# Kernel tuning notes

Hardware: AMD Instinct MI355X
Metric: run time of the kernel (lower is better)

The kernel has to match this reference:

```python
import jax, jax.numpy as jnp
import numpy as np
from jax import lax

THR = 1.0
BETA = 0.9
SLOPE = 25.0  # fast_sigmoid surrogate slope
N_JOINTS = 6

@jax.custom_vjp
def spike_fn(x):
    # Heaviside forward, fast_sigmoid surrogate backward (snntorch surrogate.fast_sigmoid)
    return (x > 0).astype(x.dtype)

def _spike_fwd(x):
    return spike_fn(x), x

def _spike_bwd(x, g):
    return (g / (SLOPE * jnp.abs(x) + 1.0) ** 2,)

spike_fn.defvjp(_spike_fwd, _spike_bwd)

def lif(cur, mem):
    # snntorch Leaky, reset_mechanism='subtract': reset from previous mem (detached)
    reset = lax.stop_gradient(spike_fn(mem - THR))
    mem = BETA * mem + cur - reset * THR
    spk = spike_fn(mem - THR)
    return spk, mem

def rate_encode(data, u):
    # data: (B, F), u: (T, B, F) uniform[0,1) -> binary spikes (T, B, F)
    dmin = jnp.min(data, axis=1, keepdims=True)
    dmax = jnp.max(data, axis=1, keepdims=True)
    rng = dmax - dmin
    rng = jnp.where(rng == 0, jnp.ones_like(rng), rng)
    norm = (data - dmin) / rng
    prob = jnp.clip(100.0 * norm * 0.001, 0.0, 1.0)  # max_rate=100, dt=0.001
    return (u < prob[None]).astype(jnp.float32)

def conv1x1(x, W, b):
    # x: (B, Cin, H, 1), W: (Cout, Cin, 1, 1)
    y = lax.conv_general_dilated(x, W, (1, 1), 'VALID',
                                 dimension_numbers=('NCHW', 'OIHW', 'NCHW'))
    return y + b[None, :, None, None]

def setup_inputs() -> dict:
    key = jax.random.key(0)
    ks = jax.random.split(key, 16)
    B, T, n = 8192, 200, N_JOINTS
    inp = {
        'x':  jax.random.normal(ks[0], (B, 3 * n), jnp.float32),
        'u1': jax.random.uniform(ks[1], (T, B, 2 * n), jnp.float32),
        'u2': jax.random.uniform(ks[2], (T, B, n), jnp.float32),
        'u3': jax.random.uniform(ks[3], (T, B, n), jnp.float32),
        'W1': jax.random.normal(ks[4], (256, 12), jnp.float32) * 0.2,
        'b1': jax.random.normal(ks[5], (256,), jnp.float32) * 0.05,
        'W2': jax.random.normal(ks[6], (256, 256), jnp.float32) * 0.06,
        'b2': jax.random.normal(ks[7], (256,), jnp.float32) * 0.05,
        'W3': jax.random.normal(ks[8], (6, 256), jnp.float32) * 0.06,
        'b3': jax.random.normal(ks[9], (6,), jnp.float32) * 0.05,
        'Wc1': jax.random.normal(ks[10], (32, 3, 1, 1), jnp.float32) * 0.5,
        'bc1': jax.random.normal(ks[11], (32,), jnp.float32) * 0.05,
        'Wc2': jax.random.normal(ks[12], (64, 32, 1, 1), jnp.float32) * 0.15,
        'bc2': jax.random.normal(ks[13], (64,), jnp.float32) * 0.05,
        'WA': jax.random.normal(ks[14], (1, 64), jnp.float32) * 0.12,
    }
    return inp

def reference(x, u1, u2, u3, W1, b1, W2, b2, W3, b3, Wc1, bc1, Wc2, bc2, WA):
    n = N_JOINTS
    B = x.shape[0]
    spk_in = rate_encode(x[:, :2 * n], u1)        # (T, B, 2n)
    spk_thdot = rate_encode(x[:, n:2 * n], u2)    # (T, B, n)
    spk_thdot2 = rate_encode(x[:, 2 * n:], u3)    # (T, B, n)

    mem1 = jnp.zeros((B, 256), jnp.float32)
    mem2 = jnp.zeros((B, 256), jnp.float32)
    mem3 = jnp.zeros((B, n), jnp.float32)
    mem4 = jnp.zeros((B, 32, n, 1), jnp.float32)
    conv_out0 = jnp.zeros((B, 64, n, 1), jnp.float32)

    def step(carry, inp):
        m1, m2, m3, m4, _ = carry
        s_in, s_td, s_td2 = inp
        spk1, m1 = lif(s_in @ W1.T + b1, m1)
        spk2, m2 = lif(spk1 @ W2.T + b2, m2)
        spk3, m3 = lif(spk2 @ W3.T + b3, m3)
        spk_conv = jnp.stack([s_td, spk3, s_td2], axis=1)[..., None]  # (B,3,n,1)
        cur4 = conv1x1(spk_conv, Wc1, bc1)  # maxpool1 with k=1 is identity
        spk4, m4 = lif(cur4, m4)
        conv_out = conv1x1(spk4, Wc2, bc2)  # maxpool2 with k=1 is identity
        return (m1, m2, m3, m4, conv_out), None

    (_, _, _, _, conv_out), _ = lax.scan(step, (mem1, mem2, mem3, mem4, conv_out0),
                                         (spk_in, spk_thdot, spk_thdot2))
    # c.T: out_a/b/c = fc_A(conv_out[:, :, i, 0]) for i in 0..2, no bias
    c_t = jnp.einsum('bcm,c->bm', conv_out[:, :, :3, 0], WA[0])  # (B, 3)
    return c_t
```

## Files before the change

### kernel.cpp

```cpp
#include <hip/hip_runtime.h>
#include <cstdint>
#include <cstddef>

typedef unsigned long long u64;

__global__ void prep_weights(const float* __restrict__ W2, const float* __restrict__ Wc2,
                             const float* __restrict__ bc2, const float* __restrict__ WA,
                             float* __restrict__ Wt2f, double* __restrict__ wEff,
                             double* __restrict__ bEff)
{
  int id = blockIdx.x * 256 + (int)threadIdx.x;
  if (id < 65536){ int i = id >> 8, j = id & 255; Wt2f[(i<<8)+j] = W2[j*256+i]; }
  else if (id < 65792){ Wt2f[id] = 0.0f; }
  if (id < 32){ double s = 0.0; for (int c=0;c<64;c++) s += (double)WA[c]*(double)Wc2[c*32+id]; wEff[id] = s; }
  if (id == 32){ double s = 0.0; for (int c=0;c<64;c++) s += (double)WA[c]*(double)bc2[c]; *bEff = s; }
}

__global__ void prep_probs(const float* __restrict__ x, double* __restrict__ probs, int B)
{
  int b = blockIdx.x, k = (int)threadIdx.x;
  if (b >= B || k >= 24) return;
  double* pb = probs + (size_t)b*24;
  if (k >= 18){ pb[k] = -1.0; return; }
  int fk, g0, gn;
  if (k < 12){ fk = k;          g0 = 0;  gn = 12; }
  else if (k < 15){ fk = 6+(k-12);  g0 = 6;  gn = 6; }
  else           { fk = 12+(k-15); g0 = 12; gn = 6; }
  const float* xb = x + (size_t)b*18;
  double mn = (double)xb[g0], mx = mn;
  for (int f = 1; f < gn; f++){ double v = (double)xb[g0+f]; mn = fmin(mn, v); mx = fmax(mx, v); }
  double rng = mx - mn; if (rng == 0.0) rng = 1.0;
  double norm = ((double)xb[fk] - mn) / rng;
  double p = (100.0 * norm) * 0.001;
  p = fmin(fmax(p, 0.0), 1.0);
  pb[k] = p;
}

__global__ void prep_enc(const float* __restrict__ u1, const float* __restrict__ u2,
                         const float* __restrict__ u3, const double* __restrict__ probs,
                         unsigned* __restrict__ encT, int B, int T)
{
  int b = blockIdx.x * blockDim.x + (int)threadIdx.x;
  int t = blockIdx.y;
  if (b >= B) return;
  if (t >= T){ encT[(size_t)b*(T+2) + t] = 0u; return; }
  const double* pb = probs + (size_t)b*24;
  size_t r = (size_t)t * B + b;
  const float* a1 = u1 + r*12;
  const float* a2 = u2 + r*6;
  const float* a3 = u3 + r*6;
  unsigned e = 0;
  #pragma unroll
  for (int k = 0; k < 12; k++) if ((double)a1[k] < pb[k])    e |= (1u << k);
  #pragma unroll
  for (int h = 0; h < 3; h++)  if ((double)a2[h] < pb[12+h]) e |= (1u << (12+h));
  #pragma unroll
  for (int h = 0; h < 3; h++)  if ((double)a3[h] < pb[15+h]) e |= (1u << (15+h));
  encT[(size_t)b*(T+2) + t] = e;
}

__global__ __launch_bounds__(256) void snn_main(
    const unsigned* __restrict__ encT,
    const float* __restrict__ b1, const float* __restrict__ b2, const float* __restrict__ b3,
    const float* __restrict__ W1, const float* __restrict__ W3,
    const float* __restrict__ Wc1, const float* __restrict__ bc1,
    const float* __restrict__ Wt2f,
    const double* __restrict__ wEff, const double* __restrict__ bEff,
    float* __restrict__ out, int B, int T)
{
  __shared__ __align__(16) float s_w1[12*256];
  __shared__ __align__(16) float s_w3[257*4];

  const int tid  = (int)threadIdx.x;
  const int lane = tid & 63;
  const int wid  = tid >> 6;
  const int b = blockIdx.x * 4 + wid;
  const int l4 = lane << 2;
  const int lcl = (lane < 3) ? lane : 3;

  for (int i = tid; i < 3072; i += 256){ int k = i >> 8, j = i & 255; s_w1[i] = W1[j*12+k]; }
  for (int i = tid; i < 1028; i += 256){
    int r = i >> 2, c = i & 3;
    s_w3[i] = (r < 256 && c < 3) ? W3[c*256 + r] : 0.0f;
  }
  __syncthreads();
  if (b >= B) return;

  const float4 b1f = *(const float4*)(b1 + l4);
  const float4 b2f = *(const float4*)(b2 + l4);
  const double b1d0=b1f.x, b1d1=b1f.y, b1d2=b1f.z, b1d3=b1f.w;
  const double b2d0=b2f.x, b2d1=b2f.y, b2d2=b2f.z, b2d3=b2f.w;
  const double b3d = (lane < 3) ? (double)b3[lane] : 0.0;
  double wc1b=0.0, wEd=0.0, pre0=0.0, pre1=0.0, pre2=0.0, pre3=0.0;
  if (lane < 32){
    double wa = (double)Wc1[lane*3+0];
    wc1b      = (double)Wc1[lane*3+1];
    double wc = (double)Wc1[lane*3+2];
    double bd = (double)bc1[lane];
    wEd  = wEff[lane];
    pre0 = bd;
    pre1 = bd + wa;
    pre2 = bd + wc;
    pre3 = bd + wa + wc;
  }

  double m10=0,m11=0,m12=0,m13=0;
  double m20=0,m21=0,m22=0,m23=0;
  double m3v=0;
  double m40=0,m41=0,m42=0;
  bool sp20=false,sp21=false,sp22=false,sp23=false;
  bool sp3v=false;
  bool sp40=false,sp41=false,sp42=false;

  const unsigned* encTb = encT + (size_t)b * (T + 2);

  unsigned e_cur = __builtin_amdgcn_readfirstlane(encTb[0]);
  unsigned e_nx  = __builtin_amdgcn_readfirstlane(encTb[1]);
  double ca0=b1d0, ca1=b1d1, ca2=b1d2, ca3=b1d3;
  {
    unsigned w = e_cur & 0xFFFu;
    while (w){
      int k = __builtin_ctz(w); w &= w-1;
      const float4 r = *(const float4*)&s_w1[(k<<8) + l4];
      ca0 += (double)r.x; ca1 += (double)r.y; ca2 += (double)r.z; ca3 += (double)r.w;
    }
  }

  for (int t = 0; t < T; t++){
    m10 = fma(0.9, m10, ca0);
    m11 = fma(0.9, m11, ca1);
    m12 = fma(0.9, m12, ca2);
    m13 = fma(0.9, m13, ca3);
    const bool sp10 = m10 > 1.0; u64 w0 = __ballot(sp10);
    const bool sp11 = m11 > 1.0; u64 w1 = __ballot(sp11);
    const bool sp12 = m12 > 1.0; u64 w2 = __ballot(sp12);
    const bool sp13 = m13 > 1.0; u64 w3m = __ballot(sp13);

    int i0 = w0  ? (((int)__builtin_ctzll(w0) <<2)|0) : 256;  w0  &= w0 -1;
    int i1 = w1  ? (((int)__builtin_ctzll(w1) <<2)|1) : 256;  w1  &= w1 -1;
    int i2 = w2  ? (((int)__builtin_ctzll(w2) <<2)|2) : 256;  w2  &= w2 -1;
    int i3 = w3m ? (((int)__builtin_ctzll(w3m)<<2)|3) : 256;  w3m &= w3m-1;
    const float4 g0 = *(const float4*)(Wt2f + ((size_t)i0<<8) + l4);
    const float4 g1 = *(const float4*)(Wt2f + ((size_t)i1<<8) + l4);
    const float4 g2 = *(const float4*)(Wt2f + ((size_t)i2<<8) + l4);
    const float4 g3 = *(const float4*)(Wt2f + ((size_t)i3<<8) + l4);

    const unsigned e_n2 = encTb[t+2];

    ca0 = (sp10 ? -1.0 : 0.0) + b1d0;
    ca1 = (sp11 ? -1.0 : 0.0) + b1d1;
    ca2 = (sp12 ? -1.0 : 0.0) + b1d2;
    ca3 = (sp13 ? -1.0 : 0.0) + b1d3;
    {
      unsigned w = e_nx & 0xFFFu;
      while (w){
        int k = __builtin_ctz(w); w &= w-1;
        const float4 r = *(const float4*)&s_w1[(k<<8) + l4];
        ca0 += (double)r.x; ca1 += (double)r.y; ca2 += (double)r.z; ca3 += (double)r.w;
      }
    }

    double c0 = (sp20 ? -1.0 : 0.0) + b2d0;
    double c1 = (sp21 ? -1.0 : 0.0) + b2d1;
    double c2 = (sp22 ? -1.0 : 0.0) + b2d2;
    double c3 = (sp23 ? -1.0 : 0.0) + b2d3;
    if (i0 != 256){ c0 += (double)g0.x; c1 += (double)g0.y; c2 += (double)g0.z; c3 += (double)g0.w; }
    if (i1 != 256){ c0 += (double)g1.x; c1 += (double)g1.y; c2 += (double)g1.z; c3 += (double)g1.w; }
    if (i2 != 256){ c0 += (double)g2.x; c1 += (double)g2.y; c2 += (double)g2.z; c3 += (double)g2.w; }
    if (i3 != 256){ c0 += (double)g3.x; c1 += (double)g3.y; c2 += (double)g3.z; c3 += (double)g3.w; }

    while (w0 | w1 | w2 | w3m){
      int j0 = w0  ? (((int)__builtin_ctzll(w0) <<2)|0) : 256;  w0  &= w0 -1;
      int j1 = w1  ? (((int)__builtin_ctzll(w1) <<2)|1) : 256;  w1  &= w1 -1;
      int j2 = w2  ? (((int)__builtin_ctzll(w2) <<2)|2) : 256;  w2  &= w2 -1;
      int j3 = w3m ? (((int)__builtin_ctzll(w3m)<<2)|3) : 256;  w3m &= w3m-1;
      const float4 h0 = *(const float4*)(Wt2f + ((size_t)j0<<8) + l4);
      const float4 h1 = *(const float4*)(Wt2f + ((size_t)j1<<8) + l4);
      const float4 h2 = *(const float4*)(Wt2f + ((size_t)j2<<8) + l4);
      const float4 h3 = *(const float4*)(Wt2f + ((size_t)j3<<8) + l4);
      if (j0 != 256){ c0 += (double)h0.x; c1 += (double)h0.y; c2 += (double)h0.z; c3 += (double)h0.w; }
      if (j1 != 256){ c0 += (double)h1.x; c1 += (double)h1.y; c2 += (double)h1.z; c3 += (double)h1.w; }
      if (j2 != 256){ c0 += (double)h2.x; c1 += (double)h2.y; c2 += (double)h2.z; c3 += (double)h2.w; }
      if (j3 != 256){ c0 += (double)h3.x; c1 += (double)h3.y; c2 += (double)h3.z; c3 += (double)h3.w; }
    }

    m20 = fma(0.9, m20, c0);
    m21 = fma(0.9, m21, c1);
    m22 = fma(0.9, m22, c2);
    m23 = fma(0.9, m23, c3);
    sp20 = m20 > 1.0; u64 v0 = __ballot(sp20);
    sp21 = m21 > 1.0; u64 v1 = __ballot(sp21);
    sp22 = m22 > 1.0; u64 v2 = __ballot(sp22);
    sp23 = m23 > 1.0; u64 v3 = __ballot(sp23);

    double cl3 = (sp3v ? -1.0 : 0.0) + b3d;
    while (v0 | v1 | v2 | v3){
      int j0 = v0 ? (((int)__builtin_ctzll(v0)<<2)|0) : 256;  v0 &= v0-1;
      int j1 = v1 ? (((int)__builtin_ctzll(v1)<<2)|1) : 256;  v1 &= v1-1;
      int j2 = v2 ? (((int)__builtin_ctzll(v2)<<2)|2) : 256;  v2 &= v2-1;
      int j3 = v3 ? (((int)__builtin_ctzll(v3)<<2)|3) : 256;  v3 &= v3-1;
      if (j0 != 256) cl3 += (double)s_w3[(j0<<2) + lcl];
      if (j1 != 256) cl3 += (double)s_w3[(j1<<2) + lcl];
      if (j2 != 256) cl3 += (double)s_w3[(j2<<2) + lcl];
      if (j3 != 256) cl3 += (double)s_w3[(j3<<2) + lcl];
    }
    m3v = fma(0.9, m3v, cl3);
    sp3v = m3v > 1.0;
    const unsigned s3 = (unsigned)(__ballot((lane < 3) && sp3v) & 7ull);

    const unsigned td  = (e_cur >> 12) & 7u;
    const unsigned td2 = (e_cur >> 15) & 7u;
    {
      double cur, t1, t2;
      t1 = (td2 & 1u) ? pre2 : pre0;  t2 = (td2 & 1u) ? pre3 : pre1;
      cur = (td & 1u) ? t2 : t1;
      if (s3 & 1u) cur += wc1b;
      cur += sp40 ? -1.0 : 0.0;
      m40 = fma(0.9, m40, cur); sp40 = m40 > 1.0;
      t1 = (td2 & 2u) ? pre2 : pre0;  t2 = (td2 & 2u) ? pre3 : pre1;
      cur = (td & 2u) ? t2 : t1;
      if (s3 & 2u) cur += wc1b;
      cur += sp41 ? -1.0 : 0.0;
      m41 = fma(0.9, m41, cur); sp41 = m41 > 1.0;
      t1 = (td2 & 4u) ? pre2 : pre0;  t2 = (td2 & 4u) ? pre3 : pre1;
      cur = (td & 4u) ? t2 : t1;
      if (s3 & 4u) cur += wc1b;
      cur += sp42 ? -1.0 : 0.0;
      m42 = fma(0.9, m42, cur); sp42 = m42 > 1.0;
    }

    e_cur = e_nx;
    e_nx  = __builtin_amdgcn_readfirstlane(e_n2);
  }

  double o0 = sp40 ? wEd : 0.0;
  double o1 = sp41 ? wEd : 0.0;
  double o2 = sp42 ? wEd : 0.0;
  for (int off = 32; off > 0; off >>= 1){
    o0 += __shfl_xor(o0, off, 64);
    o1 += __shfl_xor(o1, off, 64);
    o2 += __shfl_xor(o2, off, 64);
  }
  if (lane == 0){
    const double be = *bEff;
    out[b*3+0] = (float)(o0 + be);
    out[b*3+1] = (float)(o1 + be);
    out[b*3+2] = (float)(o2 + be);
  }
}

extern "C" void kernel_launch(void* const* d_in, const int* in_sizes, int n_in,
                              void* d_out, int out_size, void* d_ws, size_t ws_size,
                              hipStream_t stream)
{
  const float* x   = (const float*)d_in[0];
  const float* u1  = (const float*)d_in[1];
  const float* u2  = (const float*)d_in[2];
  const float* u3  = (const float*)d_in[3];
  const float* W1  = (const float*)d_in[4];
  const float* b1  = (const float*)d_in[5];
  const float* W2  = (const float*)d_in[6];
  const float* b2  = (const float*)d_in[7];
  const float* W3  = (const float*)d_in[8];
  const float* b3  = (const float*)d_in[9];
  const float* Wc1 = (const float*)d_in[10];
  const float* bc1 = (const float*)d_in[11];
  const float* Wc2 = (const float*)d_in[12];
  const float* bc2 = (const float*)d_in[13];
  const float* WA  = (const float*)d_in[14];
  float* out = (float*)d_out;

  const int B = in_sizes[0] / 18;
  const int T = in_sizes[1] / (B * 12);

  char* ws = (char*)d_ws;
  float*  Wt2f  = (float*)(ws + 0);
  double* wEff  = (double*)(ws + 263168);
  double* bEff  = (double*)(ws + 263424);
  double* probs = (double*)(ws + 263432);
  unsigned* encT= (unsigned*)(ws + 263432 + (size_t)B*24*8);

  hipLaunchKernelGGL(prep_weights, dim3(257), dim3(256), 0, stream,
                     W2, Wc2, bc2, WA, Wt2f, wEff, bEff);
  hipLaunchKernelGGL(prep_probs, dim3(B), dim3(64), 0, stream, x, probs, B);
  hipLaunchKernelGGL(prep_enc, dim3((B+255)/256, T+2), dim3(256), 0, stream,
                     u1, u2, u3, probs, encT, B, T);
  hipLaunchKernelGGL(snn_main, dim3((B+3)/4), dim3(256), 0, stream,
                     encT, b1, b2, b3, W1, W3, Wc1, bc1, Wt2f, wEff, bEff, out, B, T);
}
```

Measured before the change: 684.1 us.

## Split each batch row across two wavefronts with LDS ballot exchange

Each batch sample now runs on two wavefronts of a 128-thread block, and each lane owns two hidden neurons instead of four. The wavefronts swap their spike ballots through shared memory and block barriers twice per timestep, and only wave 0 evaluates layers 3 and 4. W1 and W3 transposes move into the prep kernel and are read from global memory instead of per-block LDS copies. This shortens the per-wave serial dependency chain and raises parallelism, at the cost of two __syncthreads per step and duplicated spike-list walks in both waves.

```diff
diff --git a/kernel.cpp b/kernel.cpp
--- a/kernel.cpp
+++ b/kernel.cpp
@@ -4,14 +4,24 @@
 
 typedef unsigned long long u64;
 
-__global__ void prep_weights(const float* __restrict__ W2, const float* __restrict__ Wc2,
+__device__ inline u64 rfl64(u64 v){
+  unsigned lo = __builtin_amdgcn_readfirstlane((unsigned)v);
+  unsigned hi = __builtin_amdgcn_readfirstlane((unsigned)(v >> 32));
+  return ((u64)hi << 32) | lo;
+}
+
+__global__ void prep_weights(const float* __restrict__ W1, const float* __restrict__ W2,
+                             const float* __restrict__ W3, const float* __restrict__ Wc2,
                              const float* __restrict__ bc2, const float* __restrict__ WA,
-                             float* __restrict__ Wt2f, double* __restrict__ wEff,
+                             float* __restrict__ Wt1g, float* __restrict__ Wt2f,
+                             float* __restrict__ Wt3f, double* __restrict__ wEff,
                              double* __restrict__ bEff)
 {
   int id = blockIdx.x * 256 + (int)threadIdx.x;
   if (id < 65536){ int i = id >> 8, j = id & 255; Wt2f[(i<<8)+j] = W2[j*256+i]; }
   else if (id < 65792){ Wt2f[id] = 0.0f; }
+  if (id < 3072){ int k = id >> 8, j = id & 255; Wt1g[(k<<8)+j] = W1[j*12+k]; }
+  if (id < 1028){ int r = id >> 2, c = id & 3; Wt3f[id] = (r < 256 && c < 3) ? W3[c*256+r] : 0.0f; }
   if (id < 32){ double s = 0.0; for (int c=0;c<64;c++) s += (double)WA[c]*(double)Wc2[c*32+id]; wEff[id] = s; }
   if (id == 32){ double s = 0.0; for (int c=0;c<64;c++) s += (double)WA[c]*(double)bc2[c]; *bEff = s; }
 }
@@ -59,40 +69,30 @@
   encT[(size_t)b*(T+2) + t] = e;
 }
 
-__global__ __launch_bounds__(256) void snn_main(
+__global__ __launch_bounds__(128, 8) void snn_main(
     const unsigned* __restrict__ encT,
     const float* __restrict__ b1, const float* __restrict__ b2, const float* __restrict__ b3,
-    const float* __restrict__ W1, const float* __restrict__ W3,
     const float* __restrict__ Wc1, const float* __restrict__ bc1,
-    const float* __restrict__ Wt2f,
+    const float* __restrict__ Wt1g, const float* __restrict__ Wt2f, const float* __restrict__ Wt3f,
     const double* __restrict__ wEff, const double* __restrict__ bEff,
     float* __restrict__ out, int B, int T)
 {
-  __shared__ __align__(16) float s_w1[12*256];
-  __shared__ __align__(16) float s_w3[257*4];
+  __shared__ u64 xb1[2][2];
+  __shared__ u64 xb2[2];
 
   const int tid  = (int)threadIdx.x;
   const int lane = tid & 63;
-  const int wid  = tid >> 6;
-  const int b = blockIdx.x * 4 + wid;
-  const int l4 = lane << 2;
-  const int lcl = (lane < 3) ? lane : 3;
-
-  for (int i = tid; i < 3072; i += 256){ int k = i >> 8, j = i & 255; s_w1[i] = W1[j*12+k]; }
-  for (int i = tid; i < 1028; i += 256){
-    int r = i >> 2, c = i & 3;
-    s_w3[i] = (r < 256 && c < 3) ? W3[c*256 + r] : 0.0f;
-  }
-  __syncthreads();
+  const int wv   = tid >> 6;
+  const int b    = blockIdx.x;
   if (b >= B) return;
-
-  const float4 b1f = *(const float4*)(b1 + l4);
-  const float4 b2f = *(const float4*)(b2 + l4);
-  const double b1d0=b1f.x, b1d1=b1f.y, b1d2=b1f.z, b1d3=b1f.w;
-  const double b2d0=b2f.x, b2d1=b2f.y, b2d2=b2f.z, b2d3=b2f.w;
+  const int j2   = (wv << 7) + (lane << 1);
+  const int lcl  = (lane < 3) ? lane : 3;
+
+  const float2 b1f = *(const float2*)(b1 + j2);
+  const float2 b2f = *(const float2*)(b2 + j2);
   const double b3d = (lane < 3) ? (double)b3[lane] : 0.0;
   double wc1b=0.0, wEd=0.0, pre0=0.0, pre1=0.0, pre2=0.0, pre3=0.0;
-  if (lane < 32){
+  if (wv == 0 && lane < 32){
     double wa = (double)Wc1[lane*3+0];
     wc1b      = (double)Wc1[lane*3+1];
     double wc = (double)Wc1[lane*3+2];
@@ -104,126 +104,132 @@
     pre3 = bd + wa + wc;
   }
 
-  double m10=0,m11=0,m12=0,m13=0;
-  double m20=0,m21=0,m22=0,m23=0;
+  double m10=0,m11=0;
+  double m20=0,m21=0;
   double m3v=0;
   double m40=0,m41=0,m42=0;
-  bool sp20=false,sp21=false,sp22=false,sp23=false;
+  bool sp20=false,sp21=false;
   bool sp3v=false;
   bool sp40=false,sp41=false,sp42=false;
 
   const unsigned* encTb = encT + (size_t)b * (T + 2);
-
   unsigned e_cur = __builtin_amdgcn_readfirstlane(encTb[0]);
   unsigned e_nx  = __builtin_amdgcn_readfirstlane(encTb[1]);
-  double ca0=b1d0, ca1=b1d1, ca2=b1d2, ca3=b1d3;
+
+  double ca0 = (double)b1f.x, ca1 = (double)b1f.y;
   {
     unsigned w = e_cur & 0xFFFu;
     while (w){
       int k = __builtin_ctz(w); w &= w-1;
-      const float4 r = *(const float4*)&s_w1[(k<<8) + l4];
-      ca0 += (double)r.x; ca1 += (double)r.y; ca2 += (double)r.z; ca3 += (double)r.w;
+      const float2 r = *(const float2*)(Wt1g + (k<<8) + j2);
+      ca0 += (double)r.x; ca1 += (double)r.y;
     }
   }
 
   for (int t = 0; t < T; t++){
     m10 = fma(0.9, m10, ca0);
     m11 = fma(0.9, m11, ca1);
-    m12 = fma(0.9, m12, ca2);
-    m13 = fma(0.9, m13, ca3);
-    const bool sp10 = m10 > 1.0; u64 w0 = __ballot(sp10);
-    const bool sp11 = m11 > 1.0; u64 w1 = __ballot(sp11);
-    const bool sp12 = m12 > 1.0; u64 w2 = __ballot(sp12);
-    const bool sp13 = m13 > 1.0; u64 w3m = __ballot(sp13);
-
-    int i0 = w0  ? (((int)__builtin_ctzll(w0) <<2)|0) : 256;  w0  &= w0 -1;
-    int i1 = w1  ? (((int)__builtin_ctzll(w1) <<2)|1) : 256;  w1  &= w1 -1;
-    int i2 = w2  ? (((int)__builtin_ctzll(w2) <<2)|2) : 256;  w2  &= w2 -1;
-    int i3 = w3m ? (((int)__builtin_ctzll(w3m)<<2)|3) : 256;  w3m &= w3m-1;
-    const float4 g0 = *(const float4*)(Wt2f + ((size_t)i0<<8) + l4);
-    const float4 g1 = *(const float4*)(Wt2f + ((size_t)i1<<8) + l4);
-    const float4 g2 = *(const float4*)(Wt2f + ((size_t)i2<<8) + l4);
-    const float4 g3 = *(const float4*)(Wt2f + ((size_t)i3<<8) + l4);
+    const bool sp10 = m10 > 1.0;
+    const bool sp11 = m11 > 1.0;
+    const u64 bb0 = __ballot(sp10);
+    const u64 bb1 = __ballot(sp11);
+
+    if (lane < 2) xb1[wv][lane] = lane ? bb1 : bb0;
+    __syncthreads();
+    const u64 o0m = rfl64(xb1[wv^1][0]);
+    const u64 o1m = rfl64(xb1[wv^1][1]);
+    u64 q0, q1, q2, q3;
+    if (wv == 0){ q0 = bb0; q1 = bb1; q2 = o0m; q3 = o1m; }
+    else        { q0 = o0m; q1 = o1m; q2 = bb0; q3 = bb1; }
+
+    int i0 = q0 ? (int)(__builtin_ctzll(q0)<<1)           : 256;  q0 &= q0-1;
+    int i1 = q1 ? (int)((__builtin_ctzll(q1)<<1)|1)       : 256;  q1 &= q1-1;
+    int i2 = q2 ? (int)((__builtin_ctzll(q2)<<1)+128)     : 256;  q2 &= q2-1;
+    int i3 = q3 ? (int)(((__builtin_ctzll(q3)<<1)|1)+128) : 256;  q3 &= q3-1;
+    const float2 g0 = *(const float2*)(Wt2f + ((size_t)i0<<8) + j2);
+    const float2 g1 = *(const float2*)(Wt2f + ((size_t)i1<<8) + j2);
+    const float2 g2 = *(const float2*)(Wt2f + ((size_t)i2<<8) + j2);
+    const float2 g3 = *(const float2*)(Wt2f + ((size_t)i3<<8) + j2);
 
     const unsigned e_n2 = encTb[t+2];
 
-    ca0 = (sp10 ? -1.0 : 0.0) + b1d0;
-    ca1 = (sp11 ? -1.0 : 0.0) + b1d1;
-    ca2 = (sp12 ? -1.0 : 0.0) + b1d2;
-    ca3 = (sp13 ? -1.0 : 0.0) + b1d3;
+    ca0 = (sp10 ? -1.0 : 0.0) + (double)b1f.x;
+    ca1 = (sp11 ? -1.0 : 0.0) + (double)b1f.y;
     {
       unsigned w = e_nx & 0xFFFu;
       while (w){
         int k = __builtin_ctz(w); w &= w-1;
-        const float4 r = *(const float4*)&s_w1[(k<<8) + l4];
-        ca0 += (double)r.x; ca1 += (double)r.y; ca2 += (double)r.z; ca3 += (double)r.w;
+        const float2 r = *(const float2*)(Wt1g + (k<<8) + j2);
+        ca0 += (double)r.x; ca1 += (double)r.y;
       }
     }
 
-    double c0 = (sp20 ? -1.0 : 0.0) + b2d0;
-    double c1 = (sp21 ? -1.0 : 0.0) + b2d1;
-    double c2 = (sp22 ? -1.0 : 0.0) + b2d2;
-    double c3 = (sp23 ? -1.0 : 0.0) + b2d3;
-    if (i0 != 256){ c0 += (double)g0.x; c1 += (double)g0.y; c2 += (double)g0.z; c3 += (double)g0.w; }
-    if (i1 != 256){ c0 += (double)g1.x; c1 += (double)g1.y; c2 += (double)g1.z; c3 += (double)g1.w; }
-    if (i2 != 256){ c0 += (double)g2.x; c1 += (double)g2.y; c2 += (double)g2.z; c3 += (double)g2.w; }
-    if (i3 != 256){ c0 += (double)g3.x; c1 += (double)g3.y; c2 += (double)g3.z; c3 += (double)g3.w; }
-
-    while (w0 | w1 | w2 | w3m){
-      int j0 = w0  ? (((int)__builtin_ctzll(w0) <<2)|0) : 256;  w0  &= w0 -1;
-      int j1 = w1  ? (((int)__builtin_ctzll(w1) <<2)|1) : 256;  w1  &= w1 -1;
-      int j2 = w2  ? (((int)__builtin_ctzll(w2) <<2)|2) : 256;  w2  &= w2 -1;
-      int j3 = w3m ? (((int)__builtin_ctzll(w3m)<<2)|3) : 256;  w3m &= w3m-1;
-      const float4 h0 = *(const float4*)(Wt2f + ((size_t)j0<<8) + l4);
-      const float4 h1 = *(const float4*)(Wt2f + ((size_t)j1<<8) + l4);
-      const float4 h2 = *(const float4*)(Wt2f + ((size_t)j2<<8) + l4);
-      const float4 h3 = *(const float4*)(Wt2f + ((size_t)j3<<8) + l4);
-      if (j0 != 256){ c0 += (double)h0.x; c1 += (double)h0.y; c2 += (double)h0.z; c3 += (double)h0.w; }
-      if (j1 != 256){ c0 += (double)h1.x; c1 += (double)h1.y; c2 += (double)h1.z; c3 += (double)h1.w; }
-      if (j2 != 256){ c0 += (double)h2.x; c1 += (double)h2.y; c2 += (double)h2.z; c3 += (double)h2.w; }
-      if (j3 != 256){ c0 += (double)h3.x; c1 += (double)h3.y; c2 += (double)h3.z; c3 += (double)h3.w; }
+    double c0 = (sp20 ? -1.0 : 0.0) + (double)b2f.x;
+    double c1 = (sp21 ? -1.0 : 0.0) + (double)b2f.y;
+    if (i0 != 256){ c0 += (double)g0.x; c1 += (double)g0.y; }
+    if (i1 != 256){ c0 += (double)g1.x; c1 += (double)g1.y; }
+    if (i2 != 256){ c0 += (double)g2.x; c1 += (double)g2.y; }
+    if (i3 != 256){ c0 += (double)g3.x; c1 += (double)g3.y; }
+
+    while (q0 | q1 | q2 | q3){
+      int j0 = q0 ? (int)(__builtin_ctzll(q0)<<1)           : 256;  q0 &= q0-1;
+      int j1 = q1 ? (int)((__builtin_ctzll(q1)<<1)|1)       : 256;  q1 &= q1-1;
+      int j2i= q2 ? (int)((__builtin_ctzll(q2)<<1)+128)     : 256;  q2 &= q2-1;
+      int j3 = q3 ? (int)(((__builtin_ctzll(q3)<<1)|1)+128) : 256;  q3 &= q3-1;
+      const float2 h0 = *(const float2*)(Wt2f + ((size_t)j0 <<8) + j2);
+      const float2 h1 = *(const float2*)(Wt2f + ((size_t)j1 <<8) + j2);
+      const float2 h2 = *(const float2*)(Wt2f + ((size_t)j2i<<8) + j2);
+      const float2 h3 = *(const float2*)(Wt2f + ((size_t)j3 <<8) + j2);
+      if (j0 != 256){ c0 += (double)h0.x; c1 += (double)h0.y; }
+      if (j1 != 256){ c0 += (double)h1.x; c1 += (double)h1.y; }
+      if (j2i!= 256){ c0 += (double)h2.x; c1 += (double)h2.y; }
+      if (j3 != 256){ c0 += (double)h3.x; c1 += (double)h3.y; }
     }
 
     m20 = fma(0.9, m20, c0);
     m21 = fma(0.9, m21, c1);
-    m22 = fma(0.9, m22, c2);
-    m23 = fma(0.9, m23, c3);
-    sp20 = m20 > 1.0; u64 v0 = __ballot(sp20);
-    sp21 = m21 > 1.0; u64 v1 = __ballot(sp21);
-    sp22 = m22 > 1.0; u64 v2 = __ballot(sp22);
-    sp23 = m23 > 1.0; u64 v3 = __ballot(sp23);
-
-    double cl3 = (sp3v ? -1.0 : 0.0) + b3d;
-    while (v0 | v1 | v2 | v3){
-      int j0 = v0 ? (((int)__builtin_ctzll(v0)<<2)|0) : 256;  v0 &= v0-1;
-      int j1 = v1 ? (((int)__builtin_ctzll(v1)<<2)|1) : 256;  v1 &= v1-1;
-      int j2 = v2 ? (((int)__builtin_ctzll(v2)<<2)|2) : 256;  v2 &= v2-1;
-      int j3 = v3 ? (((int)__builtin_ctzll(v3)<<2)|3) : 256;  v3 &= v3-1;
-      if (j0 != 256) cl3 += (double)s_w3[(j0<<2) + lcl];
-      if (j1 != 256) cl3 += (double)s_w3[(j1<<2) + lcl];
-      if (j2 != 256) cl3 += (double)s_w3[(j2<<2) + lcl];
-      if (j3 != 256) cl3 += (double)s_w3[(j3<<2) + lcl];
-    }
-    m3v = fma(0.9, m3v, cl3);
-    sp3v = m3v > 1.0;
-    const unsigned s3 = (unsigned)(__ballot((lane < 3) && sp3v) & 7ull);
-
-    const unsigned td  = (e_cur >> 12) & 7u;
-    const unsigned td2 = (e_cur >> 15) & 7u;
-    {
-      double cur, t1, t2;
-      t1 = (td2 & 1u) ? pre2 : pre0;  t2 = (td2 & 1u) ? pre3 : pre1;
-      cur = (td & 1u) ? t2 : t1;
+    sp20 = m20 > 1.0;
+    sp21 = m21 > 1.0;
+    const u64 vb0 = __ballot(sp20);
+    const u64 vb1 = __ballot(sp21);
+
+    if (wv == 1 && lane < 2) xb2[lane] = lane ? vb1 : vb0;
+    __syncthreads();
+
+    if (wv == 0){
+      u64 v0 = vb0, v1 = vb1;
+      u64 v2 = rfl64(xb2[0]);
+      u64 v3 = rfl64(xb2[1]);
+      double cl3 = (sp3v ? -1.0 : 0.0) + b3d;
+      while (v0 | v1 | v2 | v3){
+        int j0 = v0 ? (int)(__builtin_ctzll(v0)<<1)           : 256;  v0 &= v0-1;
+        int j1 = v1 ? (int)((__builtin_ctzll(v1)<<1)|1)       : 256;  v1 &= v1-1;
+        int j2i= v2 ? (int)((__builtin_ctzll(v2)<<1)+128)     : 256;  v2 &= v2-1;
+        int j3 = v3 ? (int)(((__builtin_ctzll(v3)<<1)|1)+128) : 256;  v3 &= v3-1;
+        if (j0 != 256) cl3 += (double)Wt3f[(j0 <<2) + lcl];
+        if (j1 != 256) cl3 += (double)Wt3f[(j1 <<2) + lcl];
+        if (j2i!= 256) cl3 += (double)Wt3f[(j2i<<2) + lcl];
+        if (j3 != 256) cl3 += (double)Wt3f[(j3 <<2) + lcl];
+      }
+      m3v = fma(0.9, m3v, cl3);
+      sp3v = m3v > 1.0;
+      const unsigned s3 = (unsigned)(__ballot((lane < 3) && sp3v) & 7ull);
+
+      const unsigned td  = (e_cur >> 12) & 7u;
+      const unsigned td2 = (e_cur >> 15) & 7u;
+      double cur, t1v, t2v;
+      t1v = (td2 & 1u) ? pre2 : pre0;  t2v = (td2 & 1u) ? pre3 : pre1;
+      cur = (td & 1u) ? t2v : t1v;
       if (s3 & 1u) cur += wc1b;
       cur += sp40 ? -1.0 : 0.0;
       m40 = fma(0.9, m40, cur); sp40 = m40 > 1.0;
-      t1 = (td2 & 2u) ? pre2 : pre0;  t2 = (td2 & 2u) ? pre3 : pre1;
-      cur = (td & 2u) ? t2 : t1;
+      t1v = (td2 & 2u) ? pre2 : pre0;  t2v = (td2 & 2u) ? pre3 : pre1;
+      cur = (td & 2u) ? t2v : t1v;
       if (s3 & 2u) cur += wc1b;
       cur += sp41 ? -1.0 : 0.0;
       m41 = fma(0.9, m41, cur); sp41 = m41 > 1.0;
-      t1 = (td2 & 4u) ? pre2 : pre0;  t2 = (td2 & 4u) ? pre3 : pre1;
-      cur = (td & 4u) ? t2 : t1;
+      t1v = (td2 & 4u) ? pre2 : pre0;  t2v = (td2 & 4u) ? pre3 : pre1;
+      cur = (td & 4u) ? t2v : t1v;
       if (s3 & 4u) cur += wc1b;
       cur += sp42 ? -1.0 : 0.0;
       m42 = fma(0.9, m42, cur); sp42 = m42 > 1.0;
@@ -233,19 +239,21 @@
     e_nx  = __builtin_amdgcn_readfirstlane(e_n2);
   }
 
-  double o0 = sp40 ? wEd : 0.0;
-  double o1 = sp41 ? wEd : 0.0;
-  double o2 = sp42 ? wEd : 0.0;
-  for (int off = 32; off > 0; off >>= 1){
-    o0 += __shfl_xor(o0, off, 64);
-    o1 += __shfl_xor(o1, off, 64);
-    o2 += __shfl_xor(o2, off, 64);
-  }
-  if (lane == 0){
-    const double be = *bEff;
-    out[b*3+0] = (float)(o0 + be);
-    out[b*3+1] = (float)(o1 + be);
-    out[b*3+2] = (float)(o2 + be);
+  if (wv == 0){
+    double o0 = sp40 ? wEd : 0.0;
+    double o1 = sp41 ? wEd : 0.0;
+    double o2 = sp42 ? wEd : 0.0;
+    for (int off = 32; off > 0; off >>= 1){
+      o0 += __shfl_xor(o0, off, 64);
+      o1 += __shfl_xor(o1, off, 64);
+      o2 += __shfl_xor(o2, off, 64);
+    }
+    if (lane == 0){
+      const double be = *bEff;
+      out[b*3+0] = (float)(o0 + be);
+      out[b*3+1] = (float)(o1 + be);
+      out[b*3+2] = (float)(o2 + be);
+    }
   }
 }
 
@@ -275,16 +283,18 @@
 
   char* ws = (char*)d_ws;
   float*  Wt2f  = (float*)(ws + 0);
-  double* wEff  = (double*)(ws + 263168);
-  double* bEff  = (double*)(ws + 263424);
-  double* probs = (double*)(ws + 263432);
-  unsigned* encT= (unsigned*)(ws + 263432 + (size_t)B*24*8);
+  float*  Wt1g  = (float*)(ws + 263168);
+  float*  Wt3f  = (float*)(ws + 275456);
+  double* wEff  = (double*)(ws + 279576);
+  double* bEff  = (double*)(ws + 279832);
+  double* probs = (double*)(ws + 279840);
+  unsigned* encT= (unsigned*)(ws + 279840 + (size_t)B*24*8);
 
   hipLaunchKernelGGL(prep_weights, dim3(257), dim3(256), 0, stream,
-                     W2, Wc2, bc2, WA, Wt2f, wEff, bEff);
+                     W1, W2, W3, Wc2, bc2, WA, Wt1g, Wt2f, Wt3f, wEff, bEff);
   hipLaunchKernelGGL(prep_probs, dim3(B), dim3(64), 0, stream, x, probs, B);
   hipLaunchKernelGGL(prep_enc, dim3((B+255)/256, T+2), dim3(256), 0, stream,
                      u1, u2, u3, probs, encT, B, T);
-  hipLaunchKernelGGL(snn_main, dim3((B+3)/4), dim3(256), 0, stream,
-                     encT, b1, b2, b3, W1, W3, Wc1, bc1, Wt2f, wEff, bEff, out, B, T);
-}
+  hipLaunchKernelGGL(snn_main, dim3(B), dim3(128), 0, stream,
+                     encT, b1, b2, b3, Wc1, bc1, Wt1g, Wt2f, Wt3f, wEff, bEff, out, B, T);
+}
```

Result: slower. 2.002 ms (+192.6%).

## Process two batch rows per wavefront to interleave independent recurrences

Applied to the files above, without the earlier changes.

Each wavefront now simulates two batch rows (rA and rA+half) at once, interleaving their layer updates and the gathers from the transposed W2 so independent memory loads and double-precision FMAs can overlap within one serial time loop. This targets the latency-bound dependency chain of the per-row recurrence. In exchange it roughly doubles register pressure and halves the number of wavefronts launched, which can lower occupancy. The merged gather loop runs until the row with more spikes is done, so the other row's slots sit idle.

```diff
diff --git a/kernel.cpp b/kernel.cpp
--- a/kernel.cpp
+++ b/kernel.cpp
@@ -74,7 +74,8 @@
   const int tid  = (int)threadIdx.x;
   const int lane = tid & 63;
   const int wid  = tid >> 6;
-  const int b = blockIdx.x * 4 + wid;
+  const int half = (B + 1) >> 1;
+  const int rA = blockIdx.x * 4 + wid;
   const int l4 = lane << 2;
   const int lcl = (lane < 3) ? lane : 3;
 
@@ -84,12 +85,12 @@
     s_w3[i] = (r < 256 && c < 3) ? W3[c*256 + r] : 0.0f;
   }
   __syncthreads();
-  if (b >= B) return;
+  if (rA >= half) return;
+  const int rB = rA + half;
+  const bool hasB = rB < B;
 
   const float4 b1f = *(const float4*)(b1 + l4);
   const float4 b2f = *(const float4*)(b2 + l4);
-  const double b1d0=b1f.x, b1d1=b1f.y, b1d2=b1f.z, b1d3=b1f.w;
-  const double b2d0=b2f.x, b2d1=b2f.y, b2d2=b2f.z, b2d3=b2f.w;
   const double b3d = (lane < 3) ? (double)b3[lane] : 0.0;
   double wc1b=0.0, wEd=0.0, pre0=0.0, pre1=0.0, pre2=0.0, pre3=0.0;
   if (lane < 32){
@@ -98,154 +99,210 @@
     double wc = (double)Wc1[lane*3+2];
     double bd = (double)bc1[lane];
     wEd  = wEff[lane];
-    pre0 = bd;
-    pre1 = bd + wa;
-    pre2 = bd + wc;
-    pre3 = bd + wa + wc;
-  }
-
-  double m10=0,m11=0,m12=0,m13=0;
-  double m20=0,m21=0,m22=0,m23=0;
-  double m3v=0;
-  double m40=0,m41=0,m42=0;
-  bool sp20=false,sp21=false,sp22=false,sp23=false;
-  bool sp3v=false;
-  bool sp40=false,sp41=false,sp42=false;
-
-  const unsigned* encTb = encT + (size_t)b * (T + 2);
-
-  unsigned e_cur = __builtin_amdgcn_readfirstlane(encTb[0]);
-  unsigned e_nx  = __builtin_amdgcn_readfirstlane(encTb[1]);
-  double ca0=b1d0, ca1=b1d1, ca2=b1d2, ca3=b1d3;
-  {
-    unsigned w = e_cur & 0xFFFu;
-    while (w){
-      int k = __builtin_ctz(w); w &= w-1;
-      const float4 r = *(const float4*)&s_w1[(k<<8) + l4];
-      ca0 += (double)r.x; ca1 += (double)r.y; ca2 += (double)r.z; ca3 += (double)r.w;
-    }
-  }
+    pre0 = bd; pre1 = bd + wa; pre2 = bd + wc; pre3 = bd + wa + wc;
+  }
+
+  double m10A=0,m11A=0,m12A=0,m13A=0, m20A=0,m21A=0,m22A=0,m23A=0, m3A=0, m40A=0,m41A=0,m42A=0;
+  double m10B=0,m11B=0,m12B=0,m13B=0, m20B=0,m21B=0,m22B=0,m23B=0, m3B=0, m40B=0,m41B=0,m42B=0;
+  bool s20A=false,s21A=false,s22A=false,s23A=false, s3A=false, s40A=false,s41A=false,s42A=false;
+  bool s20B=false,s21B=false,s22B=false,s23B=false, s3B=false, s40B=false,s41B=false,s42B=false;
+
+  const unsigned* ebA = encT + (size_t)rA * (T + 2);
+  const unsigned* ebB = encT + (size_t)(hasB ? rB : 0) * (T + 2);
+  unsigned eAc = __builtin_amdgcn_readfirstlane(ebA[0]);
+  unsigned eAn = __builtin_amdgcn_readfirstlane(ebA[1]);
+  unsigned eBc = __builtin_amdgcn_readfirstlane(ebB[0]);
+  unsigned eBn = __builtin_amdgcn_readfirstlane(ebB[1]);
+
+#define L1G(EMASK, CA0, CA1, CA2, CA3) { unsigned w = (EMASK) & 0xFFFu; \
+    while (w){ int k = __builtin_ctz(w); w &= w-1; \
+      const float4 r = *(const float4*)&s_w1[(k<<8) + l4]; \
+      CA0 += (double)r.x; CA1 += (double)r.y; CA2 += (double)r.z; CA3 += (double)r.w; } }
+
+  double caA0=(double)b1f.x, caA1=(double)b1f.y, caA2=(double)b1f.z, caA3=(double)b1f.w;
+  double caB0=caA0, caB1=caA1, caB2=caA2, caB3=caA3;
+  L1G(eAc, caA0, caA1, caA2, caA3)
+  L1G(eBc, caB0, caB1, caB2, caB3)
+
+#define SLOT(Wm, CW, DST) { DST = (Wm) ? (((int)__builtin_ctzll(Wm)<<2)|(CW)) : 256; Wm &= (Wm)-1; }
 
   for (int t = 0; t < T; t++){
-    m10 = fma(0.9, m10, ca0);
-    m11 = fma(0.9, m11, ca1);
-    m12 = fma(0.9, m12, ca2);
-    m13 = fma(0.9, m13, ca3);
-    const bool sp10 = m10 > 1.0; u64 w0 = __ballot(sp10);
-    const bool sp11 = m11 > 1.0; u64 w1 = __ballot(sp11);
-    const bool sp12 = m12 > 1.0; u64 w2 = __ballot(sp12);
-    const bool sp13 = m13 > 1.0; u64 w3m = __ballot(sp13);
-
-    int i0 = w0  ? (((int)__builtin_ctzll(w0) <<2)|0) : 256;  w0  &= w0 -1;
-    int i1 = w1  ? (((int)__builtin_ctzll(w1) <<2)|1) : 256;  w1  &= w1 -1;
-    int i2 = w2  ? (((int)__builtin_ctzll(w2) <<2)|2) : 256;  w2  &= w2 -1;
-    int i3 = w3m ? (((int)__builtin_ctzll(w3m)<<2)|3) : 256;  w3m &= w3m-1;
-    const float4 g0 = *(const float4*)(Wt2f + ((size_t)i0<<8) + l4);
-    const float4 g1 = *(const float4*)(Wt2f + ((size_t)i1<<8) + l4);
-    const float4 g2 = *(const float4*)(Wt2f + ((size_t)i2<<8) + l4);
-    const float4 g3 = *(const float4*)(Wt2f + ((size_t)i3<<8) + l4);
-
-    const unsigned e_n2 = encTb[t+2];
-
-    ca0 = (sp10 ? -1.0 : 0.0) + b1d0;
-    ca1 = (sp11 ? -1.0 : 0.0) + b1d1;
-    ca2 = (sp12 ? -1.0 : 0.0) + b1d2;
-    ca3 = (sp13 ? -1.0 : 0.0) + b1d3;
+    m10A = fma(0.9, m10A, caA0);  m11A = fma(0.9, m11A, caA1);
+    m12A = fma(0.9, m12A, caA2);  m13A = fma(0.9, m13A, caA3);
+    m10B = fma(0.9, m10B, caB0);  m11B = fma(0.9, m11B, caB1);
+    m12B = fma(0.9, m12B, caB2);  m13B = fma(0.9, m13B, caB3);
+    const bool p10A = m10A > 1.0; u64 wA0 = __ballot(p10A);
+    const bool p11A = m11A > 1.0; u64 wA1 = __ballot(p11A);
+    const bool p12A = m12A > 1.0; u64 wA2 = __ballot(p12A);
+    const bool p13A = m13A > 1.0; u64 wA3 = __ballot(p13A);
+    const bool p10B = m10B > 1.0; u64 wB0 = __ballot(p10B);
+    const bool p11B = m11B > 1.0; u64 wB1 = __ballot(p11B);
+    const bool p12B = m12B > 1.0; u64 wB2 = __ballot(p12B);
+    const bool p13B = m13B > 1.0; u64 wB3 = __ballot(p13B);
+
+    int iA0, iA1, iA2, iA3, iB0, iB1, iB2, iB3;
+    SLOT(wA0, 0, iA0) SLOT(wA1, 1, iA1) SLOT(wA2, 2, iA2) SLOT(wA3, 3, iA3)
+    SLOT(wB0, 0, iB0) SLOT(wB1, 1, iB1) SLOT(wB2, 2, iB2) SLOT(wB3, 3, iB3)
+    const float4 gA0 = *(const float4*)(Wt2f + ((size_t)iA0<<8) + l4);
+    const float4 gA1 = *(const float4*)(Wt2f + ((size_t)iA1<<8) + l4);
+    const float4 gA2 = *(const float4*)(Wt2f + ((size_t)iA2<<8) + l4);
+    const float4 gA3 = *(const float4*)(Wt2f + ((size_t)iA3<<8) + l4);
+    const float4 gB0 = *(const float4*)(Wt2f + ((size_t)iB0<<8) + l4);
+    const float4 gB1 = *(const float4*)(Wt2f + ((size_t)iB1<<8) + l4);
+    const float4 gB2 = *(const float4*)(Wt2f + ((size_t)iB2<<8) + l4);
+    const float4 gB3 = *(const float4*)(Wt2f + ((size_t)iB3<<8) + l4);
+
+    const unsigned eA2 = ebA[t+2];
+    const unsigned eB2 = ebB[t+2];
+
+    caA0 = (p10A ? -1.0 : 0.0) + (double)b1f.x;
+    caA1 = (p11A ? -1.0 : 0.0) + (double)b1f.y;
+    caA2 = (p12A ? -1.0 : 0.0) + (double)b1f.z;
+    caA3 = (p13A ? -1.0 : 0.0) + (double)b1f.w;
+    L1G(eAn, caA0, caA1, caA2, caA3)
+    caB0 = (p10B ? -1.0 : 0.0) + (double)b1f.x;
+    caB1 = (p11B ? -1.0 : 0.0) + (double)b1f.y;
+    caB2 = (p12B ? -1.0 : 0.0) + (double)b1f.z;
+    caB3 = (p13B ? -1.0 : 0.0) + (double)b1f.w;
+    L1G(eBn, caB0, caB1, caB2, caB3)
+
+    double cA0 = (s20A ? -1.0 : 0.0) + (double)b2f.x;
+    double cA1 = (s21A ? -1.0 : 0.0) + (double)b2f.y;
+    double cA2 = (s22A ? -1.0 : 0.0) + (double)b2f.z;
+    double cA3 = (s23A ? -1.0 : 0.0) + (double)b2f.w;
+    if (iA0 != 256){ cA0 += (double)gA0.x; cA1 += (double)gA0.y; cA2 += (double)gA0.z; cA3 += (double)gA0.w; }
+    if (iA1 != 256){ cA0 += (double)gA1.x; cA1 += (double)gA1.y; cA2 += (double)gA1.z; cA3 += (double)gA1.w; }
+    if (iA2 != 256){ cA0 += (double)gA2.x; cA1 += (double)gA2.y; cA2 += (double)gA2.z; cA3 += (double)gA2.w; }
+    if (iA3 != 256){ cA0 += (double)gA3.x; cA1 += (double)gA3.y; cA2 += (double)gA3.z; cA3 += (double)gA3.w; }
+    double cB0 = (s20B ? -1.0 : 0.0) + (double)b2f.x;
+    double cB1 = (s21B ? -1.0 : 0.0) + (double)b2f.y;
+    double cB2 = (s22B ? -1.0 : 0.0) + (double)b2f.z;
+    double cB3 = (s23B ? -1.0 : 0.0) + (double)b2f.w;
+    if (iB0 != 256){ cB0 += (double)gB0.x; cB1 += (double)gB0.y; cB2 += (double)gB0.z; cB3 += (double)gB0.w; }
+    if (iB1 != 256){ cB0 += (double)gB1.x; cB1 += (double)gB1.y; cB2 += (double)gB1.z; cB3 += (double)gB1.w; }
+    if (iB2 != 256){ cB0 += (double)gB2.x; cB1 += (double)gB2.y; cB2 += (double)gB2.z; cB3 += (double)gB2.w; }
+    if (iB3 != 256){ cB0 += (double)gB3.x; cB1 += (double)gB3.y; cB2 += (double)gB3.z; cB3 += (double)gB3.w; }
+
+    while (wA0 | wA1 | wA2 | wA3 | wB0 | wB1 | wB2 | wB3){
+      int jA0, jA1, jA2, jA3, jB0, jB1, jB2, jB3;
+      SLOT(wA0, 0, jA0) SLOT(wA1, 1, jA1) SLOT(wA2, 2, jA2) SLOT(wA3, 3, jA3)
+      SLOT(wB0, 0, jB0) SLOT(wB1, 1, jB1) SLOT(wB2, 2, jB2) SLOT(wB3, 3, jB3)
+      const float4 hA0 = *(const float4*)(Wt2f + ((size_t)jA0<<8) + l4);
+      const float4 hA1 = *(const float4*)(Wt2f + ((size_t)jA1<<8) + l4);
+      const float4 hA2 = *(const float4*)(Wt2f + ((size_t)jA2<<8) + l4);
+      const float4 hA3 = *(const float4*)(Wt2f + ((size_t)jA3<<8) + l4);
+      const float4 hB0 = *(const float4*)(Wt2f + ((size_t)jB0<<8) + l4);
+      const float4 hB1 = *(const float4*)(Wt2f + ((size_t)jB1<<8) + l4);
+      const float4 hB2 = *(const float4*)(Wt2f + ((size_t)jB2<<8) + l4);
+      const float4 hB3 = *(const float4*)(Wt2f + ((size_t)jB3<<8) + l4);
+      if (jA0 != 256){ cA0 += (double)hA0.x; cA1 += (double)hA0.y; cA2 += (double)hA0.z; cA3 += (double)hA0.w; }
+      if (jA1 != 256){ cA0 += (double)hA1.x; cA1 += (double)hA1.y; cA2 += (double)hA1.z; cA3 += (double)hA1.w; }
+      if (jA2 != 256){ cA0 += (double)hA2.x; cA1 += (double)hA2.y; cA2 += (double)hA2.z; cA3 += (double)hA2.w; }
+      if (jA3 != 256){ cA0 += (double)hA3.x; cA1 += (double)hA3.y; cA2 += (double)hA3.z; cA3 += (double)hA3.w; }
+      if (jB0 != 256){ cB0 += (double)hB0.x; cB1 += (double)hB0.y; cB2 += (double)hB0.z; cB3 += (double)hB0.w; }
+      if (jB1 != 256){ cB0 += (double)hB1.x; cB1 += (double)hB1.y; cB2 += (double)hB1.z; cB3 += (double)hB1.w; }
+      if (jB2 != 256){ cB0 += (double)hB2.x; cB1 += (double)hB2.y; cB2 += (double)hB2.z; cB3 += (double)hB2.w; }
+      if (jB3 != 256){ cB0 += (double)hB3.x; cB1 += (double)hB3.y; cB2 += (double)hB3.z; cB3 += (double)hB3.w; }
+    }
+
+    m20A = fma(0.9, m20A, cA0);  m21A = fma(0.9, m21A, cA1);
+    m22A = fma(0.9, m22A, cA2);  m23A = fma(0.9, m23A, cA3);
+    m20B = fma(0.9, m20B, cB0);  m21B = fma(0.9, m21B, cB1);
+    m22B = fma(0.9, m22B, cB2);  m23B = fma(0.9, m23B, cB3);
+    s20A = m20A > 1.0; u64 vA0 = __ballot(s20A);
+    s21A = m21A > 1.0; u64 vA1 = __ballot(s21A);
+    s22A = m22A > 1.0; u64 vA2 = __ballot(s22A);
+    s23A = m23A > 1.0; u64 vA3 = __ballot(s23A);
+    s20B = m20B > 1.0; u64 vB0 = __ballot(s20B);
+    s21B = m21B > 1.0; u64 vB1 = __ballot(s21B);
+    s22B = m22B > 1.0; u64 vB2 = __ballot(s22B);
+    s23B = m23B > 1.0; u64 vB3 = __ballot(s23B);
+
+    double cl3A = (s3A ? -1.0 : 0.0) + b3d;
+    while (vA0 | vA1 | vA2 | vA3){
+      int j0, j1, j2, j3;
+      SLOT(vA0, 0, j0) SLOT(vA1, 1, j1) SLOT(vA2, 2, j2) SLOT(vA3, 3, j3)
+      if (j0 != 256) cl3A += (double)s_w3[(j0<<2) + lcl];
+      if (j1 != 256) cl3A += (double)s_w3[(j1<<2) + lcl];
+      if (j2 != 256) cl3A += (double)s_w3[(j2<<2) + lcl];
+      if (j3 != 256) cl3A += (double)s_w3[(j3<<2) + lcl];
+    }
+    m3A = fma(0.9, m3A, cl3A);
+    s3A = m3A > 1.0;
+    const unsigned q3A = (unsigned)(__ballot((lane < 3) && s3A) & 7ull);
+
+    double cl3B = (s3B ? -1.0 : 0.0) + b3d;
+    while (vB0 | vB1 | vB2 | vB3){
+      int j0, j1, j2, j3;
+      SLOT(vB0, 0, j0) SLOT(vB1, 1, j1) SLOT(vB2, 2, j2) SLOT(vB3, 3, j3)
+      if (j0 != 256) cl3B += (double)s_w3[(j0<<2) + lcl];
+      if (j1 != 256) cl3B += (double)s_w3[(j1<<2) + lcl];
+      if (j2 != 256) cl3B += (double)s_w3[(j2<<2) + lcl];
+      if (j3 != 256) cl3B += (double)s_w3[(j3<<2) + lcl];
+    }
+    m3B = fma(0.9, m3B, cl3B);
+    s3B = m3B > 1.0;
+    const unsigned q3B = (unsigned)(__ballot((lane < 3) && s3B) & 7ull);
+
     {
-      unsigned w = e_nx & 0xFFFu;
-      while (w){
-        int k = __builtin_ctz(w); w &= w-1;
-        const float4 r = *(const float4*)&s_w1[(k<<8) + l4];
-        ca0 += (double)r.x; ca1 += (double)r.y; ca2 += (double)r.z; ca3 += (double)r.w;
-      }
-    }
-
-    double c0 = (sp20 ? -1.0 : 0.0) + b2d0;
-    double c1 = (sp21 ? -1.0 : 0.0) + b2d1;
-    double c2 = (sp22 ? -1.0 : 0.0) + b2d2;
-    double c3 = (sp23 ? -1.0 : 0.0) + b2d3;
-    if (i0 != 256){ c0 += (double)g0.x; c1 += (double)g0.y; c2 += (double)g0.z; c3 += (double)g0.w; }
-    if (i1 != 256){ c0 += (double)g1.x; c1 += (double)g1.y; c2 += (double)g1.z; c3 += (double)g1.w; }
-    if (i2 != 256){ c0 += (double)g2.x; c1 += (double)g2.y; c2 += (double)g2.z; c3 += (double)g2.w; }
-    if (i3 != 256){ c0 += (double)g3.x; c1 += (double)g3.y; c2 += (double)g3.z; c3 += (double)g3.w; }
-
-    while (w0 | w1 | w2 | w3m){
-      int j0 = w0  ? (((int)__builtin_ctzll(w0) <<2)|0) : 256;  w0  &= w0 -1;
-      int j1 = w1  ? (((int)__builtin_ctzll(w1) <<2)|1) : 256;  w1  &= w1 -1;
-      int j2 = w2  ? (((int)__builtin_ctzll(w2) <<2)|2) : 256;  w2  &= w2 -1;
-      int j3 = w3m ? (((int)__builtin_ctzll(w3m)<<2)|3) : 256;  w3m &= w3m-1;
-      const float4 h0 = *(const float4*)(Wt2f + ((size_t)j0<<8) + l4);
-      const float4 h1 = *(const float4*)(Wt2f + ((size_t)j1<<8) + l4);
-      const float4 h2 = *(const float4*)(Wt2f + ((size_t)j2<<8) + l4);
-      const float4 h3 = *(const float4*)(Wt2f + ((size_t)j3<<8) + l4);
-      if (j0 != 256){ c0 += (double)h0.x; c1 += (double)h0.y; c2 += (double)h0.z; c3 += (double)h0.w; }
-      if (j1 != 256){ c0 += (double)h1.x; c1 += (double)h1.y; c2 += (double)h1.z; c3 += (double)h1.w; }
-      if (j2 != 256){ c0 += (double)h2.x; c1 += (double)h2.y; c2 += (double)h2.z; c3 += (double)h2.w; }
-      if (j3 != 256){ c0 += (double)h3.x; c1 += (double)h3.y; c2 += (double)h3.z; c3 += (double)h3.w; }
-    }
-
-    m20 = fma(0.9, m20, c0);
-    m21 = fma(0.9, m21, c1);
-    m22 = fma(0.9, m22, c2);
-    m23 = fma(0.9, m23, c3);
-    sp20 = m20 > 1.0; u64 v0 = __ballot(sp20);
-    sp21 = m21 > 1.0; u64 v1 = __ballot(sp21);
-    sp22 = m22 > 1.0; u64 v2 = __ballot(sp22);
-    sp23 = m23 > 1.0; u64 v3 = __ballot(sp23);
-
-    double cl3 = (sp3v ? -1.0 : 0.0) + b3d;
-    while (v0 | v1 | v2 | v3){
-      int j0 = v0 ? (((int)__builtin_ctzll(v0)<<2)|0) : 256;  v0 &= v0-1;
-      int j1 = v1 ? (((int)__builtin_ctzll(v1)<<2)|1) : 256;  v1 &= v1-1;
-      int j2 = v2 ? (((int)__builtin_ctzll(v2)<<2)|2) : 256;  v2 &= v2-1;
-      int j3 = v3 ? (((int)__builtin_ctzll(v3)<<2)|3) : 256;  v3 &= v3-1;
-      if (j0 != 256) cl3 += (double)s_w3[(j0<<2) + lcl];
-      if (j1 != 256) cl3 += (double)s_w3[(j1<<2) + lcl];
-      if (j2 != 256) cl3 += (double)s_w3[(j2<<2) + lcl];
-      if (j3 != 256) cl3 += (double)s_w3[(j3<<2) + lcl];
-    }
-    m3v = fma(0.9, m3v, cl3);
-    sp3v = m3v > 1.0;
-    const unsigned s3 = (unsigned)(__ballot((lane < 3) && sp3v) & 7ull);
-
-    const unsigned td  = (e_cur >> 12) & 7u;
-    const unsigned td2 = (e_cur >> 15) & 7u;
-    {
+      const unsigned td  = (eAc >> 12) & 7u;
+      const unsigned td2 = (eAc >> 15) & 7u;
       double cur, t1, t2;
       t1 = (td2 & 1u) ? pre2 : pre0;  t2 = (td2 & 1u) ? pre3 : pre1;
-      cur = (td & 1u) ? t2 : t1;
-      if (s3 & 1u) cur += wc1b;
-      cur += sp40 ? -1.0 : 0.0;
-      m40 = fma(0.9, m40, cur); sp40 = m40 > 1.0;
+      cur = (td & 1u) ? t2 : t1;  if (q3A & 1u) cur += wc1b;  cur += s40A ? -1.0 : 0.0;
+      m40A = fma(0.9, m40A, cur); s40A = m40A > 1.0;
       t1 = (td2 & 2u) ? pre2 : pre0;  t2 = (td2 & 2u) ? pre3 : pre1;
-      cur = (td & 2u) ? t2 : t1;
-      if (s3 & 2u) cur += wc1b;
-      cur += sp41 ? -1.0 : 0.0;
-      m41 = fma(0.9, m41, cur); sp41 = m41 > 1.0;
+      cur = (td & 2u) ? t2 : t1;  if (q3A & 2u) cur += wc1b;  cur += s41A ? -1.0 : 0.0;
+      m41A = fma(0.9, m41A, cur); s41A = m41A > 1.0;
       t1 = (td2 & 4u) ? pre2 : pre0;  t2 = (td2 & 4u) ? pre3 : pre1;
-      cur = (td & 4u) ? t2 : t1;
-      if (s3 & 4u) cur += wc1b;
-      cur += sp42 ? -1.0 : 0.0;
-      m42 = fma(0.9, m42, cur); sp42 = m42 > 1.0;
-    }
-
-    e_cur = e_nx;
-    e_nx  = __builtin_amdgcn_readfirstlane(e_n2);
-  }
-
-  double o0 = sp40 ? wEd : 0.0;
-  double o1 = sp41 ? wEd : 0.0;
-  double o2 = sp42 ? wEd : 0.0;
-  for (int off = 32; off > 0; off >>= 1){
-    o0 += __shfl_xor(o0, off, 64);
-    o1 += __shfl_xor(o1, off, 64);
-    o2 += __shfl_xor(o2, off, 64);
-  }
-  if (lane == 0){
-    const double be = *bEff;
-    out[b*3+0] = (float)(o0 + be);
-    out[b*3+1] = (float)(o1 + be);
-    out[b*3+2] = (float)(o2 + be);
+      cur = (td & 4u) ? t2 : t1;  if (q3A & 4u) cur += wc1b;  cur += s42A ? -1.0 : 0.0;
+      m42A = fma(0.9, m42A, cur); s42A = m42A > 1.0;
+    }
+    {
+      const unsigned td  = (eBc >> 12) & 7u;
+      const unsigned td2 = (eBc >> 15) & 7u;
+      double cur, t1, t2;
+      t1 = (td2 & 1u) ? pre2 : pre0;  t2 = (td2 & 1u) ? pre3 : pre1;
+      cur = (td & 1u) ? t2 : t1;  if (q3B & 1u) cur += wc1b;  cur += s40B ? -1.0 : 0.0;
+      m40B = fma(0.9, m40B, cur); s40B = m40B > 1.0;
+      t1 = (td2 & 2u) ? pre2 : pre0;  t2 = (td2 & 2u) ? pre3 : pre1;
+      cur = (td & 2u) ? t2 : t1;  if (q3B & 2u) cur += wc1b;  cur += s41B ? -1.0 : 0.0;
+      m41B = fma(0.9, m41B, cur); s41B = m41B > 1.0;
+      t1 = (td2 & 4u) ? pre2 : pre0;  t2 = (td2 & 4u) ? pre3 : pre1;
+      cur = (td & 4u) ? t2 : t1;  if (q3B & 4u) cur += wc1b;  cur += s42B ? -1.0 : 0.0;
+      m42B = fma(0.9, m42B, cur); s42B = m42B > 1.0;
+    }
+
+    eAc = eAn;  eAn = __builtin_amdgcn_readfirstlane(eA2);
+    eBc = eBn;  eBn = __builtin_amdgcn_readfirstlane(eB2);
+  }
+
+  const double be = *bEff;
+  {
+    double o0 = s40A ? wEd : 0.0, o1 = s41A ? wEd : 0.0, o2 = s42A ? wEd : 0.0;
+    for (int off = 32; off > 0; off >>= 1){
+      o0 += __shfl_xor(o0, off, 64);
+      o1 += __shfl_xor(o1, off, 64);
+      o2 += __shfl_xor(o2, off, 64);
+    }
+    if (lane == 0){
+      out[rA*3+0] = (float)(o0 + be);
+      out[rA*3+1] = (float)(o1 + be);
+      out[rA*3+2] = (float)(o2 + be);
+    }
+  }
+  if (hasB){
+    double o0 = s40B ? wEd : 0.0, o1 = s41B ? wEd : 0.0, o2 = s42B ? wEd : 0.0;
+    for (int off = 32; off > 0; off >>= 1){
+      o0 += __shfl_xor(o0, off, 64);
+      o1 += __shfl_xor(o1, off, 64);
+      o2 += __shfl_xor(o2, off, 64);
+    }
+    if (lane == 0){
+      out[rB*3+0] = (float)(o0 + be);
+      out[rB*3+1] = (float)(o1 + be);
+      out[rB*3+2] = (float)(o2 + be);
+    }
   }
 }
 
@@ -285,6 +342,7 @@
   hipLaunchKernelGGL(prep_probs, dim3(B), dim3(64), 0, stream, x, probs, B);
   hipLaunchKernelGGL(prep_enc, dim3((B+255)/256, T+2), dim3(256), 0, stream,
                      u1, u2, u3, probs, encT, B, T);
-  hipLaunchKernelGGL(snn_main, dim3((B+3)/4), dim3(256), 0, stream,
+  const int half = (B + 1) >> 1;
+  hipLaunchKernelGGL(snn_main, dim3((half+3)/4), dim3(256), 0, stream,
                      encT, b1, b2, b3, W1, W3, Wc1, bc1, Wt2f, wEff, bEff, out, B, T);
 }
```

Measured after the change: 941.3 us. +37.6%, slower.
